# Kernel tuning notes

Hardware: AMD Instinct MI355X
Metric: run time of the kernel (lower is better)

Reference implementation:

```python
import jax, jax.numpy as jnp
import numpy as np

B_SZ, SEQ, IN, HID, MEM_D, ORDER = 64, 512, 512, 1024, 8, 256
THETA = 512.0


def _legendre_ab(order, theta):
    # Continuous-time Legendre delay system (Voelker et al.):
    # A[i,j] = (2i+1)/theta * (-1 if i<j else (-1)^(i-j+1));  B[i] = (2i+1)/theta * (-1)^i
    q = jnp.arange(order, dtype=jnp.float32)
    r = (2.0 * q + 1.0) / theta
    i, j = jnp.meshgrid(q, q, indexing='ij')
    a = jnp.where(i < j, -1.0, jnp.where(((i - j) % 2) == 1, 1.0, -1.0)) * r[:, None]
    b = jnp.where((q % 2) == 0, 1.0, -1.0) * r
    # ZOH discretization with dt=1 via augmented matrix exponential
    M = jnp.zeros((order + 1, order + 1), dtype=jnp.float32)
    M = M.at[:order, :order].set(a).at[:order, order].set(b)
    Md = jax.scipy.linalg.expm(M)
    return Md[:order, :order], Md[:order, order]


def setup_inputs() -> dict:
    key = jax.random.key(0)
    ks = jax.random.split(key, 7)
    def n(k, shape, s):
        return jax.random.normal(k, shape, dtype=jnp.float32) * jnp.float32(s)
    return {
        'x':   n(ks[0], (B_SZ, SEQ, IN), 1.0),
        'e_x': n(ks[1], (MEM_D, IN), 1.0 / np.sqrt(IN)),          # lecun_uniform_-like scale
        'e_h': n(ks[2], (MEM_D, HID), 1.0 / np.sqrt(HID)),
        'e_m': jnp.zeros((MEM_D, MEM_D * ORDER), dtype=jnp.float32),  # init_em = zeros_
        'W_x': n(ks[4], (HID, IN), np.sqrt(2.0 / (HID + IN))),    # xavier_normal_
        'W_h': n(ks[5], (HID, HID), np.sqrt(2.0 / (HID + HID))),
        'W_m': n(ks[6], (HID, MEM_D * ORDER), np.sqrt(2.0 / (HID + MEM_D * ORDER))),
    }


def reference(x, e_x, e_h, e_m, W_x, W_h, W_m):
    A, Bv = _legendre_ab(ORDER, THETA)
    bsz = x.shape[0]

    def step(carry, x_t):
        h, m = carry                      # h: [B,HID], m: [B,MEM_D,ORDER]
        m_flat = m.reshape(bsz, -1)
        # u_t = e_x x_t + e_h h_{t-1} + e_m m_{t-1}  -> [B, MEM_D]
        u = x_t @ e_x.T + h @ e_h.T + m_flat @ e_m.T
        # m_t = A m_{t-1} + B u_t (per memory channel)
        m = jnp.einsum('bdo,po->bdp', m, A) + u[:, :, None] * Bv
        m_flat = m.reshape(bsz, -1)
        # h_t = tanh(W_x x_t + W_h h_{t-1} + W_m m_t)
        h = jnp.tanh(x_t @ W_x.T + h @ W_h.T + m_flat @ W_m.T)
        return (h, m), h

    h0 = jnp.zeros((bsz, HID), dtype=x.dtype)
    m0 = jnp.zeros((bsz, MEM_D, ORDER), dtype=x.dtype)
    (_, _), ys = jax.lax.scan(step, (h0, m0), jnp.swapaxes(x, 0, 1))
    return jnp.swapaxes(ys, 0, 1)          # [B, SEQ, HID]
```

## Files before the change

kernel.cpp:

```cpp
#include <hip/hip_runtime.h>
#include <cmath>
#include <vector>

#define B_SZ 64
#define SEQ 512
#define IN_D 512
#define HID 1024
#define MEM_DIM 8
#define ORD 256
#define MFLAT 2048
#define KTOT 3584
#define NH 128
#define NM 64
#define NBLK (NH + NM)
#define BAR_STRIDE 16
#define RING 64
#define SSLOT ((size_t)B_SZ * KTOT)

typedef __attribute__((ext_vector_type(8))) short short8v;
typedef __attribute__((ext_vector_type(4))) float f32x4;
typedef unsigned long long u64;

__device__ __host__ inline unsigned short f2bf(float f) {
  union { float f; unsigned u; } v; v.f = f;
  unsigned r = v.u + 0x7FFF + ((v.u >> 16) & 1);
  return (unsigned short)(r >> 16);
}
__device__ __host__ inline float bf2f(unsigned short h) {
  union { unsigned u; float f; } v; v.u = ((unsigned)h) << 16;
  return v.f;
}

static void matmul_d(const double* A, const double* B, double* C, int n) {
  for (int i = 0; i < n; ++i) {
    double* Ci = C + (size_t)i * n;
    for (int j = 0; j < n; ++j) Ci[j] = 0.0;
    const double* Ai = A + (size_t)i * n;
    for (int k = 0; k < n; ++k) {
      double a = Ai[k];
      const double* Bk = B + (size_t)k * n;
      for (int j = 0; j < n; ++j) Ci[j] += a * Bk[j];
    }
  }
}

static void compute_AB_host(float* AdT, float* Anat, float* Bd) {
  const int q = ORD, n = ORD + 1;
  const double theta = 512.0;
  std::vector<double> M((size_t)n * n, 0.0);
  for (int i = 0; i < q; ++i) {
    double r = (2.0 * i + 1.0) / theta;
    for (int j = 0; j < q; ++j) {
      double v = (i < j) ? -1.0 : ((((i - j) % 2) == 1) ? 1.0 : -1.0);
      M[(size_t)i * n + j] = v * r;
    }
    M[(size_t)i * n + q] = (((i % 2) == 0) ? 1.0 : -1.0) * r;
  }
  double norm = 0.0;
  for (int j = 0; j < n; ++j) {
    double s = 0.0;
    for (int i = 0; i < n; ++i) s += fabs(M[(size_t)i * n + j]);
    if (s > norm) norm = s;
  }
  int s = 0;
  while (norm > 0.25) { norm *= 0.5; ++s; }
  double sc = ldexp(1.0, -s);
  for (size_t i = 0; i < M.size(); ++i) M[i] *= sc;
  std::vector<double> E((size_t)n * n, 0.0), P = M, T((size_t)n * n);
  for (int i = 0; i < n; ++i) E[(size_t)i * n + i] = 1.0;
  for (size_t i = 0; i < M.size(); ++i) E[i] += M[i];
  for (int k = 2; k <= 30; ++k) {
    matmul_d(P.data(), M.data(), T.data(), n);
    double inv = 1.0 / (double)k, mx = 0.0;
    for (size_t i = 0; i < T.size(); ++i) {
      T[i] *= inv;
      double a = fabs(T[i]);
      if (a > mx) mx = a;
    }
    P.swap(T);
    for (size_t i = 0; i < M.size(); ++i) E[i] += P[i];
    if (mx < 1e-19) break;
  }
  for (int it = 0; it < s; ++it) {
    matmul_d(E.data(), E.data(), T.data(), n);
    E.swap(T);
  }
  for (int p = 0; p < q; ++p) {
    for (int o = 0; o < q; ++o) {
      float v = (float)E[(size_t)p * n + o];
      AdT[(size_t)o * q + p] = v;
      Anat[(size_t)p * q + o] = v;
    }
    Bd[p] = (float)E[(size_t)p * n + q];
  }
}

__global__ __launch_bounds__(256) void k_wmb(const float* __restrict__ Wm,
                                             const float* __restrict__ Bd,
                                             float* __restrict__ WmB) {
  int i = blockIdx.x;
  int d = threadIdx.x >> 5, l = threadIdx.x & 31;
  const float* wr = Wm + (size_t)i * MFLAT + d * ORD;
  float acc = 0.f;
  #pragma unroll
  for (int j = 0; j < 8; ++j) { int p = l + 32 * j; acc += wr[p] * Bd[p]; }
  for (int off = 16; off; off >>= 1) acc += __shfl_xor(acc, off);
  if (l == 0) WmB[i * 8 + d] = acc;
}

__global__ __launch_bounds__(256) void k_gcat(
    const float* __restrict__ Wx, const float* __restrict__ Wh,
    const float* __restrict__ Wm, const float* __restrict__ Ex,
    const float* __restrict__ Eh, const float* __restrict__ Em,
    const float* __restrict__ Anat, const float* __restrict__ WmB,
    unsigned short* __restrict__ Ghi, unsigned short* __restrict__ Glo) {
  __shared__ float wm[MFLAT];
  __shared__ float wb[8];
  int i = blockIdx.x, tid = threadIdx.x;
  for (int k = tid; k < MFLAT; k += 256) wm[k] = Wm[(size_t)i * MFLAT + k];
  if (tid < 8) wb[tid] = WmB[i * 8 + tid];
  __syncthreads();
  unsigned short* grh = Ghi + (size_t)i * KTOT;
  unsigned short* grl = Glo + (size_t)i * KTOT;
  for (int c = tid; c < KTOT; c += 256) {
    float v;
    if (c < IN_D) {
      v = Wx[(size_t)i * IN_D + c];
      #pragma unroll
      for (int d = 0; d < 8; ++d) v += wb[d] * Ex[(size_t)d * IN_D + c];
    } else if (c < IN_D + HID) {
      int j = c - IN_D;
      v = Wh[(size_t)i * HID + j];
      #pragma unroll
      for (int d = 0; d < 8; ++d) v += wb[d] * Eh[(size_t)d * HID + j];
    } else {
      int cm = c - IN_D - HID;
      int dd = cm >> 8, o = cm & 255;
      v = 0.f;
      const float* wmd = wm + dd * ORD;
      for (int p = 0; p < ORD; ++p) v += wmd[p] * Anat[(size_t)p * ORD + o];
      #pragma unroll
      for (int d = 0; d < 8; ++d) v += wb[d] * Em[(size_t)d * MFLAT + cm];
    }
    unsigned short hi = f2bf(v);
    grh[c] = hi;
    grl[c] = f2bf(v - bf2f(hi));
  }
}

__device__ inline void grid_barrier(unsigned* __restrict__ arr,
                                    unsigned* __restrict__ go, unsigned ep,
                                    bool inv) {
  __syncthreads();
  if (blockIdx.x == 0) {
    int tid = threadIdx.x;
    if (tid > 0 && tid < NBLK) {
      while (__hip_atomic_load(&arr[tid * BAR_STRIDE], __ATOMIC_RELAXED,
                               __HIP_MEMORY_SCOPE_AGENT) < ep)
        __builtin_amdgcn_s_sleep(1);
    }
    __syncthreads();
    if (tid == 0)
      __hip_atomic_store(go, ep, __ATOMIC_RELEASE, __HIP_MEMORY_SCOPE_AGENT);
  } else {
    if (threadIdx.x == 0) {
      __hip_atomic_store(&arr[blockIdx.x * BAR_STRIDE], ep, __ATOMIC_RELEASE,
                         __HIP_MEMORY_SCOPE_AGENT);
      while (__hip_atomic_load(go, __ATOMIC_RELAXED,
                               __HIP_MEMORY_SCOPE_AGENT) < ep)
        __builtin_amdgcn_s_sleep(1);
    }
  }
  if (inv && threadIdx.x == 0)
    __builtin_amdgcn_fence(__ATOMIC_ACQUIRE, "agent");
  __syncthreads();
}

__global__ __launch_bounds__(256) void k_persist(
    const float* __restrict__ x, const float* __restrict__ Ex,
    const float* __restrict__ Eh, const float* __restrict__ Em,
    const unsigned short* __restrict__ Ghi, const unsigned short* __restrict__ Glo,
    const float* __restrict__ AdT, const float* __restrict__ Bd,
    unsigned short* __restrict__ shR, unsigned short* __restrict__ slR,
    float* __restrict__ mfp0, float* __restrict__ mfp1,
    float* __restrict__ out, unsigned* __restrict__ barArr,
    unsigned* __restrict__ barGo) {
  int tid = threadIdx.x;
  unsigned ep = 0;

  if (blockIdx.x < NH) {
    __shared__ float hx[2][64][4];
    int s = blockIdx.x & 7, sub = blockIdx.x >> 3;
    int isub = sub & 3, bq = sub >> 2;
    int w = tid >> 6, lane = tid & 63;
    int tw = w & 1, kh = w >> 1;
    int b0 = bq * 16;
    int i0 = s * 128 + isub * 32 + tw * 16;
    size_t aoff = (size_t)(b0 + (lane & 15)) * KTOT + (lane >> 4) * 8;
    const unsigned short* bh_ = Ghi + (size_t)(i0 + (lane & 15)) * KTOT + (lane >> 4) * 8;
    const unsigned short* bl_ = Glo + (size_t)(i0 + (lane & 15)) * KTOT + (lane >> 4) * 8;

    grid_barrier(barArr, barGo, ++ep, false);

    for (int t = 0; t < SEQ; ++t) {
      const unsigned short* ah_ = shR + (size_t)(t & (RING - 1)) * SSLOT + aoff;
      const unsigned short* al_ = slR + (size_t)(t & (RING - 1)) * SSLOT + aoff;
      unsigned short* snh = shR + (size_t)((t + 1) & (RING - 1)) * SSLOT;
      unsigned short* snl = slR + (size_t)((t + 1) & (RING - 1)) * SSLOT;

      f32x4 ahh = {0.f,0.f,0.f,0.f}, alh = {0.f,0.f,0.f,0.f}, ahl = {0.f,0.f,0.f,0.f};
      int kbase = kh * 1792;
      #pragma unroll 4
      for (int kk = 0; kk < 56; ++kk) {
        int k = kbase + kk * 32;
        short8v avh = *(const short8v*)(ah_ + k);
        short8v avl = *(const short8v*)(al_ + k);
        short8v bvh = *(const short8v*)(bh_ + k);
        short8v bvl = *(const short8v*)(bl_ + k);
        ahh = __builtin_amdgcn_mfma_f32_16x16x32_bf16(avh, bvh, ahh, 0, 0, 0);
        alh = __builtin_amdgcn_mfma_f32_16x16x32_bf16(avl, bvh, alh, 0, 0, 0);
        ahl = __builtin_amdgcn_mfma_f32_16x16x32_bf16(avh, bvl, ahl, 0, 0, 0);
      }
      f32x4 acc = ahh + alh + ahl;
      if (kh == 1) {
        *(f32x4*)&hx[tw][lane][0] = acc;
      }
      __syncthreads();
      if (kh == 0) {
        f32x4 o4 = *(const f32x4*)&hx[tw][lane][0];
        #pragma unroll
        for (int r = 0; r < 4; ++r) {
          float v = acc[r] + o4[r];
          float hv = tanhf(v);
          int b = b0 + (lane >> 4) * 4 + r;
          int i = i0 + (lane & 15);
          unsigned short hi = f2bf(hv);
          snh[(size_t)b * KTOT + IN_D + i] = hi;
          snl[(size_t)b * KTOT + IN_D + i] = f2bf(hv - bf2f(hi));
          __builtin_nontemporal_store(hv, &out[((size_t)b * SEQ + t) * HID + i]);
        }
      }
      grid_barrier(barArr, barGo, ++ep, (t & 31) == 31);
    }
  } else {
    __shared__ float sst[KTOT];
    __shared__ float mpart[4][MFLAT];
    __shared__ float ush[8];
    int b = blockIdx.x - NH;
    int du = tid >> 5, lu = tid & 31;
    const float* exr = Ex + (size_t)du * IN_D;
    const float* ehr = Eh + (size_t)du * HID;
    const float* emr = Em + (size_t)du * MFLAT;
    int os = tid >> 6;
    int p0 = (tid & 63) * 4;
    int dp0 = tid * 8;
    int dr = tid >> 5;
    float bdv[8];
    #pragma unroll
    for (int j = 0; j < 8; ++j) bdv[j] = Bd[(dp0 & 255) + j];

    {
      const float* xr = x + (size_t)b * SEQ * IN_D;
      for (int k = tid; k < IN_D; k += 256) {
        float xv = xr[k];
        unsigned short hi = f2bf(xv);
        shR[(size_t)b * KTOT + k] = hi;
        slR[(size_t)b * KTOT + k] = f2bf(xv - bf2f(hi));
      }
    }
    grid_barrier(barArr, barGo, ++ep, false);

    for (int t = 0; t < SEQ; ++t) {
      const unsigned short* scH = shR + (size_t)(t & (RING - 1)) * SSLOT;
      const unsigned short* scL = slR + (size_t)(t & (RING - 1)) * SSLOT;
      unsigned short* snh = shR + (size_t)((t + 1) & (RING - 1)) * SSLOT;
      unsigned short* snl = slR + (size_t)((t + 1) & (RING - 1)) * SSLOT;
      const float* mc = (t & 1) ? mfp1 : mfp0;
      float* mn = (t & 1) ? mfp0 : mfp1;

      const float* xrow = x + ((size_t)b * SEQ + t) * IN_D;
      #pragma unroll
      for (int j = 0; j < 2; ++j) {
        int k = tid + 256 * j;
        sst[k] = xrow[k];
      }
      {
        int k4 = tid * 4;
        const unsigned short* hh = scH + (size_t)b * KTOT + IN_D + k4;
        const unsigned short* hl = scL + (size_t)b * KTOT + IN_D + k4;
        #pragma unroll
        for (int j = 0; j < 4; ++j)
          sst[IN_D + k4 + j] = bf2f(hh[j]) + bf2f(hl[j]);
      }
      {
        const float4* mc4 = (const float4*)(mc + (size_t)b * MFLAT);
        float4* sst4 = (float4*)(sst + IN_D + HID);
        #pragma unroll
        for (int j = 0; j < 2; ++j) {
          int g = tid + 256 * j;
          sst4[g] = mc4[g];
        }
      }
      __syncthreads();

      float ua = 0.f;
      #pragma unroll 4
      for (int j = 0; j < 16; ++j) { int k = lu + 32 * j; ua += exr[k] * sst[k]; }
      #pragma unroll 4
      for (int j = 0; j < 32; ++j) { int k = lu + 32 * j; ua += ehr[k] * sst[IN_D + k]; }
      #pragma unroll 4
      for (int j = 0; j < 64; ++j) { int k = lu + 32 * j; ua += emr[k] * sst[IN_D + HID + k]; }
      #pragma unroll
      for (int off = 16; off; off >>= 1) ua += __shfl_xor(ua, off);
      if (lu == 0) ush[du] = ua;
      __syncthreads();

      float acc[8][4];
      #pragma unroll
      for (int d = 0; d < 8; ++d)
        acc[d][0] = acc[d][1] = acc[d][2] = acc[d][3] = 0.f;
      const float* mbase = sst + IN_D + HID;
      #pragma unroll 4
      for (int oo = 0; oo < 64; ++oo) {
        int o = os * 64 + oo;
        float4 qv = *(const float4*)(AdT + (size_t)o * ORD + p0);
        #pragma unroll
        for (int d = 0; d < 8; ++d) {
          float mv = mbase[d * ORD + o];
          acc[d][0] = fmaf(qv.x, mv, acc[d][0]);
          acc[d][1] = fmaf(qv.y, mv, acc[d][1]);
          acc[d][2] = fmaf(qv.z, mv, acc[d][2]);
          acc[d][3] = fmaf(qv.w, mv, acc[d][3]);
        }
      }
      #pragma unroll
      for (int d = 0; d < 8; ++d)
        *(float4*)&mpart[os][d * ORD + p0] =
            make_float4(acc[d][0], acc[d][1], acc[d][2], acc[d][3]);
      __syncthreads();

      float r[8];
      float uv = ush[dr];
      #pragma unroll
      for (int j = 0; j < 8; ++j) r[j] = bdv[j] * uv;
      #pragma unroll
      for (int sI = 0; sI < 4; ++sI) {
        float4 v0 = *(const float4*)&mpart[sI][dp0];
        float4 v1 = *(const float4*)&mpart[sI][dp0 + 4];
        r[0] += v0.x; r[1] += v0.y; r[2] += v0.z; r[3] += v0.w;
        r[4] += v1.x; r[5] += v1.y; r[6] += v1.z; r[7] += v1.w;
      }
      float4* mo4 = (float4*)(mn + (size_t)b * MFLAT + dp0);
      mo4[0] = make_float4(r[0], r[1], r[2], r[3]);
      mo4[1] = make_float4(r[4], r[5], r[6], r[7]);
      unsigned short ph[8], pl[8];
      #pragma unroll
      for (int j = 0; j < 8; ++j) {
        ph[j] = f2bf(r[j]);
        pl[j] = f2bf(r[j] - bf2f(ph[j]));
      }
      size_t moff = (size_t)b * KTOT + IN_D + HID + dp0;
      *(short8v*)(snh + moff) = *(short8v*)ph;
      *(short8v*)(snl + moff) = *(short8v*)pl;

      if (t + 1 < SEQ) {
        const float* xn = x + ((size_t)b * SEQ + t + 1) * IN_D;
        for (int k = tid; k < IN_D; k += 256) {
          float xv = xn[k];
          unsigned short hi = f2bf(xv);
          snh[(size_t)b * KTOT + k] = hi;
          snl[(size_t)b * KTOT + k] = f2bf(xv - bf2f(hi));
        }
      }
      __syncthreads();
      grid_barrier(barArr, barGo, ++ep, (t & 31) == 31);
    }
  }
}

extern "C" void kernel_launch(void* const* d_in, const int* in_sizes, int n_in,
                              void* d_out, int out_size, void* d_ws, size_t ws_size,
                              hipStream_t stream) {
  const float* x  = (const float*)d_in[0];
  const float* Ex = (const float*)d_in[1];
  const float* Eh = (const float*)d_in[2];
  const float* Em = (const float*)d_in[3];
  const float* Wx = (const float*)d_in[4];
  const float* Wh = (const float*)d_in[5];
  const float* Wm = (const float*)d_in[6];
  float* out = (float*)d_out;
  float* ws = (float*)d_ws;

  float* dAnat = ws;
  float* dAdT  = dAnat + 65536;
  float* dBd   = dAdT + 65536;
  float* dWmB  = dBd + 512;
  unsigned short* dGhi = (unsigned short*)(dWmB + 8192);
  unsigned short* dGlo = dGhi + (size_t)HID * KTOT;
  unsigned short* shR  = dGlo + (size_t)HID * KTOT;
  unsigned short* slR  = shR + (size_t)RING * SSLOT;
  float* mfp0 = (float*)(slR + (size_t)RING * SSLOT);
  float* mfp1 = mfp0 + B_SZ * MFLAT;
  unsigned* barArr  = (unsigned*)(mfp1 + B_SZ * MFLAT);
  unsigned* barGo   = barArr + NBLK * BAR_STRIDE;

  static float h_AdT[ORD * ORD];
  static float h_Anat[ORD * ORD];
  static float h_Bd[ORD];
  compute_AB_host(h_AdT, h_Anat, h_Bd);
  hipMemcpyAsync(dAdT,  h_AdT,  sizeof(h_AdT),  hipMemcpyHostToDevice, stream);
  hipMemcpyAsync(dAnat, h_Anat, sizeof(h_Anat), hipMemcpyHostToDevice, stream);
  hipMemcpyAsync(dBd,   h_Bd,   sizeof(h_Bd),   hipMemcpyHostToDevice, stream);

  hipMemsetAsync(shR, 0, SSLOT * sizeof(unsigned short), stream);
  hipMemsetAsync(slR, 0, SSLOT * sizeof(unsigned short), stream);
  hipMemsetAsync(mfp0, 0, (size_t)B_SZ * MFLAT * sizeof(float), stream);
  hipMemsetAsync(barArr, 0,
                 (size_t)(NBLK * BAR_STRIDE + BAR_STRIDE) * sizeof(unsigned), stream);

  k_wmb<<<dim3(HID), dim3(256), 0, stream>>>(Wm, dBd, dWmB);
  k_gcat<<<dim3(HID), dim3(256), 0, stream>>>(Wx, Wh, Wm, Ex, Eh, Em, dAnat, dWmB, dGhi, dGlo);

  k_persist<<<dim3(NBLK), dim3(256), 0, stream>>>(
      x, Ex, Eh, Em, dGhi, dGlo, dAdT, dBd, shR, slR,
      mfp0, mfp1, out, barArr, barGo);
}
```

Baseline: 17.92 ms.

## Double hidden-state blocks and split K four ways per block

Doubles the number of persistent blocks computing the hidden-state GEMM from 128 to 256. Each block now owns one 16x16 output tile and splits the K dimension across its four waves instead of two. Partial sums are reduced through shared memory, and every thread finishes one output element. The intent is to shorten the serial per-step GEMM latency by spreading it over more CUs, at the cost of more blocks joining each grid barrier and a larger barrier poll loop in block 0.

Result: slower. 53.49 ms (+198.4%).

```diff
diff --git a/kernel.cpp b/kernel.cpp
--- a/kernel.cpp
+++ b/kernel.cpp
@@ -10,7 +10,7 @@
 #define ORD 256
 #define MFLAT 2048
 #define KTOT 3584
-#define NH 128
+#define NH 256
 #define NM 64
 #define NBLK (NH + NM)
 #define BAR_STRIDE 16
@@ -154,10 +154,12 @@
   __syncthreads();
   if (blockIdx.x == 0) {
     int tid = threadIdx.x;
-    if (tid > 0 && tid < NBLK) {
-      while (__hip_atomic_load(&arr[tid * BAR_STRIDE], __ATOMIC_RELAXED,
-                               __HIP_MEMORY_SCOPE_AGENT) < ep)
-        __builtin_amdgcn_s_sleep(1);
+    for (int sI = tid; sI < NBLK; sI += 256) {
+      if (sI > 0) {
+        while (__hip_atomic_load(&arr[sI * BAR_STRIDE], __ATOMIC_RELAXED,
+                                 __HIP_MEMORY_SCOPE_AGENT) < ep)
+          __builtin_amdgcn_s_sleep(1);
+      }
     }
     __syncthreads();
     if (tid == 0)
@@ -189,16 +191,16 @@
   unsigned ep = 0;
 
   if (blockIdx.x < NH) {
-    __shared__ float hx[2][64][4];
-    int s = blockIdx.x & 7, sub = blockIdx.x >> 3;
-    int isub = sub & 3, bq = sub >> 2;
+    __shared__ float part[4][256];
+    int s = blockIdx.x & 7, u = blockIdx.x >> 3;
+    int it = u & 7, bq = u >> 3;
     int w = tid >> 6, lane = tid & 63;
-    int tw = w & 1, kh = w >> 1;
     int b0 = bq * 16;
-    int i0 = s * 128 + isub * 32 + tw * 16;
+    int i0 = s * 128 + it * 16;
     size_t aoff = (size_t)(b0 + (lane & 15)) * KTOT + (lane >> 4) * 8;
     const unsigned short* bh_ = Ghi + (size_t)(i0 + (lane & 15)) * KTOT + (lane >> 4) * 8;
     const unsigned short* bl_ = Glo + (size_t)(i0 + (lane & 15)) * KTOT + (lane >> 4) * 8;
+    int kbase = w * 896;
 
     grid_barrier(barArr, barGo, ++ep, false);
 
@@ -209,9 +211,8 @@
       unsigned short* snl = slR + (size_t)((t + 1) & (RING - 1)) * SSLOT;
 
       f32x4 ahh = {0.f,0.f,0.f,0.f}, alh = {0.f,0.f,0.f,0.f}, ahl = {0.f,0.f,0.f,0.f};
-      int kbase = kh * 1792;
       #pragma unroll 4
-      for (int kk = 0; kk < 56; ++kk) {
+      for (int kk = 0; kk < 28; ++kk) {
         int k = kbase + kk * 32;
         short8v avh = *(const short8v*)(ah_ + k);
         short8v avl = *(const short8v*)(al_ + k);
@@ -222,23 +223,19 @@
         ahl = __builtin_amdgcn_mfma_f32_16x16x32_bf16(avh, bvl, ahl, 0, 0, 0);
       }
       f32x4 acc = ahh + alh + ahl;
-      if (kh == 1) {
-        *(f32x4*)&hx[tw][lane][0] = acc;
-      }
+      #pragma unroll
+      for (int r = 0; r < 4; ++r)
+        part[w][((lane >> 4) * 4 + r) * 16 + (lane & 15)] = acc[r];
       __syncthreads();
-      if (kh == 0) {
-        f32x4 o4 = *(const f32x4*)&hx[tw][lane][0];
-        #pragma unroll
-        for (int r = 0; r < 4; ++r) {
-          float v = acc[r] + o4[r];
-          float hv = tanhf(v);
-          int b = b0 + (lane >> 4) * 4 + r;
-          int i = i0 + (lane & 15);
-          unsigned short hi = f2bf(hv);
-          snh[(size_t)b * KTOT + IN_D + i] = hi;
-          snl[(size_t)b * KTOT + IN_D + i] = f2bf(hv - bf2f(hi));
-          __builtin_nontemporal_store(hv, &out[((size_t)b * SEQ + t) * HID + i]);
-        }
+      {
+        float v = part[0][tid] + part[1][tid] + part[2][tid] + part[3][tid];
+        float hv = tanhf(v);
+        int b = b0 + (tid >> 4);
+        int i = i0 + (tid & 15);
+        unsigned short hi = f2bf(hv);
+        snh[(size_t)b * KTOT + IN_D + i] = hi;
+        snl[(size_t)b * KTOT + IN_D + i] = f2bf(hv - bf2f(hi));
+        __builtin_nontemporal_store(hv, &out[((size_t)b * SEQ + t) * HID + i]);
       }
       grid_barrier(barArr, barGo, ++ep, (t & 31) == 31);
     }
```
